# Optimization experiments

Hardware: AMD Instinct MI355X
Metric: run time of the kernel (lower is better)

The kernel has to match this reference:

```python
import jax, jax.numpy as jnp
import numpy as np

# Module hyperparameters (from init_kwargs)
LATENT = 1024
H = 16          # num query heads
HK = 4          # num key/value heads (GQA)
D = 64          # head_dim
CAUSAL = True
QKV_OUT = (3 * H + 2 * HK) * D  # 3584, as defined in the source module


def setup_inputs() -> dict:
    key = jax.random.key(0)
    k1, k2, k3 = jax.random.split(key, 3)
    B, S = 2, 2048
    x = jax.random.normal(k1, (B, S, LATENT), dtype=jnp.float32)
    # nn.Linear weights are [out_features, in_features]; scale like torch default init
    w_qkv = jax.random.normal(k2, (QKV_OUT, LATENT), dtype=jnp.float32) / np.sqrt(LATENT)
    w_out = jax.random.normal(k3, (LATENT, H * D), dtype=jnp.float32) / np.sqrt(H * D)
    return {"x": x, "w_qkv": w_qkv, "w_out": w_out}


def reference(x, w_qkv, w_out):
    B, S, _ = x.shape
    scale = 1.0 / np.sqrt(D).astype(np.float32)

    # Fused QKV projection: [B,S,(3H+2HK)*D]
    qkv = jnp.einsum('bsl,ol->bso', x, w_qkv)

    # Split: q takes H heads, k and v take HK heads each (GQA).
    # (The extra 2*H*D columns of the fused projection are allocated by the
    #  source module but unused by q/k/v, matching its layer sizing.)
    q = qkv[..., : H * D].reshape(B, S, H, D)
    k = qkv[..., H * D:(H + HK) * D].reshape(B, S, HK, D)
    v = qkv[..., (H + HK) * D:(H + 2 * HK) * D].reshape(B, S, HK, D)

    # Expand KV heads to match query heads (group factor H // HK)
    rep = H // HK
    k = jnp.repeat(k, rep, axis=2)  # [B,S,H,D]
    v = jnp.repeat(v, rep, axis=2)

    # Scaled dot-product attention
    scores = jnp.einsum('bshd,bthd->bhst', q, k) * scale  # [B,H,S,S]
    if CAUSAL:
        causal_mask = jnp.tril(jnp.ones((S, S), dtype=bool))
        scores = jnp.where(causal_mask, scores, jnp.finfo(scores.dtype).min)
    attn = jax.nn.softmax(scores, axis=-1)
    out = jnp.einsum('bhst,bthd->bshd', attn, v).reshape(B, S, H * D)

    # Output projection back to latent_size
    return jnp.einsum('bso,lo->bsl', out, w_out)
```

## Files before the change

### kernel.cpp

```cpp
#include <hip/hip_runtime.h>
#include <hip/hip_bf16.h>
#include <math.h>

typedef __attribute__((ext_vector_type(8))) short bf16x8;
typedef __attribute__((ext_vector_type(4))) float f32x4;
typedef unsigned short u16;
typedef unsigned int   u32;

#define DEVINL __device__ __forceinline__

DEVINL u16 f2bf(float x) {
    u32 u = __float_as_uint(x);
    u += 0x7fffu + ((u >> 16) & 1u);
    return (u16)(u >> 16);
}

DEVINL void gl_lds16(const void* g, void* s) {
    __builtin_amdgcn_global_load_lds(
        (const __attribute__((address_space(1))) u32*)g,
        (__attribute__((address_space(3))) u32*)s,
        16, 0, 0);
}

DEVINL f32x4 mfma16(bf16x8 a, bf16x8 b, f32x4 c) {
    return __builtin_amdgcn_mfma_f32_16x16x32_bf16(a, b, c, 0, 0, 0);
}

__global__ void cvt3(const float* __restrict__ x, const float* __restrict__ wq,
                     const float* __restrict__ wo,
                     u16* __restrict__ xb, u16* __restrict__ wqb, u16* __restrict__ wob) {
    int i = blockIdx.x * 256 + threadIdx.x;
    const float* s; u16* d; int j;
    if (i < 1048576)      { s = x;  d = xb;  j = i; }
    else if (i < 1441792) { s = wq; d = wqb; j = i - 1048576; }
    else                  { s = wo; d = wob; j = i - 1441792; }
    float4 v = ((const float4*)s)[j];
    ushort4 o;
    o.x = f2bf(v.x); o.y = f2bf(v.y); o.z = f2bf(v.z); o.w = f2bf(v.w);
    ((ushort4*)d)[j] = o;
}

template<int EP>
__launch_bounds__(256)
__global__ void gemm128(const u16* __restrict__ A, const u16* __restrict__ B,
                        const int N, const int K,
                        float* __restrict__ Cf,
                        u16* __restrict__ Qo, u16* __restrict__ Ko, u16* __restrict__ Vo)
{
    __shared__ __align__(16) u16 As[2][128 * 64];
    __shared__ __align__(16) u16 Bs[2][128 * 64];
    const int tid  = threadIdx.x;
    const int lane = tid & 63;
    const int quad = lane >> 4;
    const int lcol = lane & 15;
    const int w    = tid >> 6;
    const int wr   = w >> 1, wc = w & 1;
    const int lr   = lane >> 3;
    const int lc   = lane & 7;
    const int swst = lc ^ lr;
    const int rk   = lcol & 7;
    const int m0 = blockIdx.y * 128;
    const int n0 = blockIdx.x * 128;

    f32x4 acc[4][4];
    for (int mb = 0; mb < 4; mb++)
        for (int nb = 0; nb < 4; nb++)
            for (int i = 0; i < 4; i++) acc[mb][nb][i] = 0.f;

    const u16* Ap = A + (m0 + w * 8 + lr) * K + swst * 8;
    const u16* Bp = B + (n0 + w * 8 + lr) * K + swst * 8;

    for (int j = 0; j < 4; j++) {
        gl_lds16(Ap + j * 32 * K, &As[0][(j * 32 + w * 8) * 64]);
        gl_lds16(Bp + j * 32 * K, &Bs[0][(j * 32 + w * 8) * 64]);
    }
    __syncthreads();

    int cur = 0;
    for (int k0 = 0; k0 < K; k0 += 64) {
        if (k0 + 64 < K) {
            for (int j = 0; j < 4; j++) {
                gl_lds16(Ap + j * 32 * K + k0 + 64, &As[cur ^ 1][(j * 32 + w * 8) * 64]);
                gl_lds16(Bp + j * 32 * K + k0 + 64, &Bs[cur ^ 1][(j * 32 + w * 8) * 64]);
            }
        }
        for (int ks = 0; ks < 2; ks++) {
            const int ch = ((ks * 4 + quad) ^ rk) * 8;
            bf16x8 af[4], bf[4];
            for (int mb = 0; mb < 4; mb++)
                af[mb] = *(const bf16x8*)&As[cur][(wr * 64 + mb * 16 + lcol) * 64 + ch];
            for (int nb = 0; nb < 4; nb++)
                bf[nb] = *(const bf16x8*)&Bs[cur][(wc * 64 + nb * 16 + lcol) * 64 + ch];
            for (int mb = 0; mb < 4; mb++)
                for (int nb = 0; nb < 4; nb++)
                    acc[mb][nb] = mfma16(af[mb], bf[nb], acc[mb][nb]);
        }
        __syncthreads();
        cur ^= 1;
    }

    if (EP == 0) {
        for (int mb = 0; mb < 4; mb++)
            for (int nb = 0; nb < 4; nb++) {
                int row = m0 + wr * 64 + mb * 16 + quad * 4;
                int col = n0 + wc * 64 + nb * 16 + lcol;
                for (int i = 0; i < 4; i++)
                    Cf[(row + i) * N + col] = acc[mb][nb][i];
            }
    } else {
        const float qsc = 0.18033688011112042f;
        for (int mb = 0; mb < 4; mb++)
            for (int nb = 0; nb < 4; nb++)
                for (int i = 0; i < 4; i++) {
                    int row = m0 + wr * 64 + mb * 16 + quad * 4 + i;
                    int col = n0 + wc * 64 + nb * 16 + lcol;
                    int bb = row >> 11, ss = row & 2047;
                    if (col < 1024) {
                        int hh = col >> 6, dd = col & 63;
                        Qo[((bb * 16 + hh) * 2048 + ss) * 64 + dd] = f2bf(acc[mb][nb][i] * qsc);
                    } else if (col < 1280) {
                        int c = col - 1024, hh = c >> 6, dd = c & 63;
                        Ko[((bb * 4 + hh) * 2048 + ss) * 64 + dd] = f2bf(acc[mb][nb][i]);
                    } else {
                        int c = col - 1280, hh = c >> 6, dd = c & 63;
                        Vo[((bb * 4 + hh) * 64 + dd) * 2048 + ss] = f2bf(acc[mb][nb][i]);
                    }
                }
    }
}

__launch_bounds__(512, 4)
__global__ void attn_kernel(const u16* __restrict__ Qg, const u16* __restrict__ Kg,
                            const u16* __restrict__ Vtg, u16* __restrict__ Og)
{
    __shared__ __align__(16) u16 Ks[2][2][64 * 64];
    __shared__ __align__(16) u16 Vs[2][2][64 * 64];
    __shared__ __align__(16) u16 Ps[2][64 * 64];

    const int tid  = threadIdx.x;
    const int lane = tid & 63;
    const int w8   = tid >> 6;
    const int gpp  = w8 >> 2;
    const int wg   = w8 & 3;
    const int quad = lane >> 4;
    const int lcol = lane & 15;
    const int lr   = lane >> 3;
    const int lc   = lane & 7;
    const int swst = lc ^ lr;
    const int rk   = lcol & 7;
    const int hl   = lcol >> 3;

    const int p  = blockIdx.x;
    const int h  = blockIdx.y;
    const int b  = blockIdx.z;
    const int hk = h >> 2;

    const u16* Qp = Qg  + (b * 16 + h) * 2048 * 64;
    const u16* Kp = Kg  + (b * 4 + hk) * 2048 * 64;
    const u16* Vp = Vtg + (b * 4 + hk) * 64 * 2048;

    const int p0 = (wg * 16 + quad * 4) * 64 + ((hl ^ ((quad & 1) << 2)) << 3) + lc;

    float* Ob = (float*)(&Ks[1][0][0]);
    float* Lb = (float*)(&Vs[1][0][0]);

    for (int pass = 0; pass < 2; pass++) {
        const int qi = pass ? (31 - p) : p;
        const int q0 = qi * 64;
        const int nt = qi + 1;
        const int nIter = (nt + 1) >> 1;

        bf16x8 aqr[2];
        for (int ks = 0; ks < 2; ks++)
            aqr[ks] = *(const bf16x8*)(Qp + (q0 + wg * 16 + lcol) * 64 + ks * 32 + quad * 8);

        if (gpp < nt) {
            for (int j = 0; j < 2; j++) {
                const int r = wg * 16 + j * 8 + lr;
                gl_lds16(Kp + (gpp * 64 + r) * 64 + swst * 8, &Ks[gpp][0][wg * 1024 + j * 512]);
                gl_lds16(Vp + r * 2048 + gpp * 64 + swst * 8, &Vs[gpp][0][wg * 1024 + j * 512]);
            }
        }

        f32x4 o[4];
        float l_p[4];
        for (int db = 0; db < 4; db++)
            for (int i = 0; i < 4; i++) o[db][i] = 0.f;
        for (int i = 0; i < 4; i++) l_p[i] = 0.f;

        __syncthreads();

        for (int it = 0; it < nIter; ++it) {
            const int cur = it & 1;
            const int ti  = 2 * it + gpp;
            const int tin = ti + 2;
            if (tin < nt) {
                const int nbuf = cur ^ 1;
                for (int j = 0; j < 2; j++) {
                    const int r = wg * 16 + j * 8 + lr;
                    gl_lds16(Kp + (tin * 64 + r) * 64 + swst * 8, &Ks[gpp][nbuf][wg * 1024 + j * 512]);
                    gl_lds16(Vp + r * 2048 + tin * 64 + swst * 8, &Vs[gpp][nbuf][wg * 1024 + j * 512]);
                }
            }
            if (ti < nt) {
                f32x4 s[4];
                for (int cb = 0; cb < 4; cb++)
                    for (int i = 0; i < 4; i++) s[cb][i] = 0.f;
                for (int ks = 0; ks < 2; ks++) {
                    const int chq = ((ks * 4 + quad) ^ rk) * 8;
                    for (int cb = 0; cb < 4; cb++) {
                        bf16x8 bk = *(const bf16x8*)&Ks[gpp][cur][(cb * 16 + lcol) * 64 + chq];
                        s[cb] = mfma16(aqr[ks], bk, s[cb]);
                    }
                }

                if (ti == nt - 1) {
                    for (int cb = 0; cb < 4; cb++)
                        for (int i = 0; i < 4; i++) {
                            const bool masked = (cb * 16 + lcol) > (wg * 16 + quad * 4 + i);
                            s[cb][i] = masked ? -INFINITY : s[cb][i];
                        }
                }

                for (int cb = 0; cb < 4; cb++)
                    for (int i = 0; i < 4; i++) {
                        const float pv = __builtin_amdgcn_exp2f(s[cb][i]);
                        s[cb][i] = pv;
                        l_p[i] += pv;
                    }

                for (int cb = 0; cb < 4; cb++)
                    for (int i = 0; i < 4; i++)
                        Ps[gpp][(p0 + i * 64) ^ (((cb * 2) ^ i) << 3)] =
                            (u16)(__float_as_uint(s[cb][i]) >> 16);

                for (int kt = 0; kt < 2; kt++) {
                    const int chp = ((kt * 4 + quad) ^ rk) * 8;
                    bf16x8 ap = *(const bf16x8*)&Ps[gpp][(wg * 16 + lcol) * 64 + chp];
                    for (int db = 0; db < 4; db++) {
                        bf16x8 bv = *(const bf16x8*)&Vs[gpp][cur][(db * 16 + lcol) * 64 + chp];
                        o[db] = mfma16(ap, bv, o[db]);
                    }
                }
            }
            __syncthreads();
        }

        float lrow[4];
        for (int i = 0; i < 4; i++) {
            float l = l_p[i];
            for (int x = 1; x < 16; x <<= 1) l += __shfl_xor(l, x);
            lrow[i] = l;
        }
        if (gpp == 1) {
            for (int i = 0; i < 4; i++) {
                const int row = wg * 16 + quad * 4 + i;
                for (int db = 0; db < 4; db++)
                    Ob[row * 64 + db * 16 + lcol] = o[db][i];
                if (lcol == 0) Lb[row] = lrow[i];
            }
        }
        __syncthreads();
        if (gpp == 0) {
            for (int i = 0; i < 4; i++) {
                const int row = wg * 16 + quad * 4 + i;
                const float inv = 1.0f / (lrow[i] + Lb[row]);
                const int srow = q0 + row;
                for (int db = 0; db < 4; db++) {
                    const float val = (o[db][i] + Ob[row * 64 + db * 16 + lcol]) * inv;
                    Og[(b * 2048 + srow) * 1024 + h * 64 + db * 16 + lcol] = f2bf(val);
                }
            }
        }
        __syncthreads();
    }
}

extern "C" void kernel_launch(void* const* d_in, const int* in_sizes, int n_in,
                              void* d_out, int out_size, void* d_ws, size_t ws_size,
                              hipStream_t stream) {
    const float* x     = (const float*)d_in[0];
    const float* w_qkv = (const float*)d_in[1];
    const float* w_out = (const float*)d_in[2];
    float* out = (float*)d_out;
    char* ws = (char*)d_ws;

    u16* xb  = (u16*)(ws);
    u16* wqb = (u16*)(ws + 8  * 1024 * 1024);
    u16* wob = (u16*)(ws + 11 * 1024 * 1024);
    u16* qb  = (u16*)(ws + 13 * 1024 * 1024);
    u16* kb  = (u16*)(ws + 21 * 1024 * 1024);
    u16* vtb = (u16*)(ws + 23 * 1024 * 1024);
    u16* aob = (u16*)(ws);

    cvt3<<<6656, 256, 0, stream>>>(x, w_qkv, w_out, xb, wqb, wob);

    gemm128<1><<<dim3(12, 32), 256, 0, stream>>>(xb, wqb, 1536, 1024,
                                                 nullptr, qb, kb, vtb);
    attn_kernel<<<dim3(16, 16, 2), 512, 0, stream>>>(qb, kb, vtb, aob);
    gemm128<0><<<dim3(8, 32), 256, 0, stream>>>(aob, wob, 1024, 1024,
                                                out, nullptr, nullptr, nullptr);
}
```

Measured before the change: 165.2 us.

## Shrink GEMM tiles to 64x128 with two waves and prioritize attention MFMAs

Both projection GEMMs now use 64x128 output tiles computed by 128-thread blocks of two waves, each wave owning a 64x64 sub-tile. This doubles the grid (768 and 512 blocks) to fill the 256 CUs better, at the cost of more redundant B-tile loads per output element. The attention kernel also raises wave priority around its two MFMA loops with s_setprio, aiming to overlap matrix work with the softmax and load phases of other waves.

```diff
diff --git a/kernel.cpp b/kernel.cpp
--- a/kernel.cpp
+++ b/kernel.cpp
@@ -41,25 +41,24 @@
 }
 
 template<int EP>
-__launch_bounds__(256)
-__global__ void gemm128(const u16* __restrict__ A, const u16* __restrict__ B,
-                        const int N, const int K,
-                        float* __restrict__ Cf,
-                        u16* __restrict__ Qo, u16* __restrict__ Ko, u16* __restrict__ Vo)
+__launch_bounds__(128)
+__global__ void gemm2w(const u16* __restrict__ A, const u16* __restrict__ B,
+                       const int N, const int K,
+                       float* __restrict__ Cf,
+                       u16* __restrict__ Qo, u16* __restrict__ Ko, u16* __restrict__ Vo)
 {
-    __shared__ __align__(16) u16 As[2][128 * 64];
+    __shared__ __align__(16) u16 As[2][64 * 64];
     __shared__ __align__(16) u16 Bs[2][128 * 64];
     const int tid  = threadIdx.x;
     const int lane = tid & 63;
+    const int w    = tid >> 6;
     const int quad = lane >> 4;
     const int lcol = lane & 15;
-    const int w    = tid >> 6;
-    const int wr   = w >> 1, wc = w & 1;
     const int lr   = lane >> 3;
     const int lc   = lane & 7;
     const int swst = lc ^ lr;
     const int rk   = lcol & 7;
-    const int m0 = blockIdx.y * 128;
+    const int m0 = blockIdx.y * 64;
     const int n0 = blockIdx.x * 128;
 
     f32x4 acc[4][4];
@@ -70,30 +69,30 @@
     const u16* Ap = A + (m0 + w * 8 + lr) * K + swst * 8;
     const u16* Bp = B + (n0 + w * 8 + lr) * K + swst * 8;
 
-    for (int j = 0; j < 4; j++) {
-        gl_lds16(Ap + j * 32 * K, &As[0][(j * 32 + w * 8) * 64]);
-        gl_lds16(Bp + j * 32 * K, &Bs[0][(j * 32 + w * 8) * 64]);
-    }
+    for (int j = 0; j < 4; j++)
+        gl_lds16(Ap + j * 16 * K, &As[0][(j * 16 + w * 8) * 64]);
+    for (int g = 0; g < 8; g++)
+        gl_lds16(Bp + g * 16 * K, &Bs[0][(g * 16 + w * 8) * 64]);
     __syncthreads();
 
     int cur = 0;
     for (int k0 = 0; k0 < K; k0 += 64) {
         if (k0 + 64 < K) {
-            for (int j = 0; j < 4; j++) {
-                gl_lds16(Ap + j * 32 * K + k0 + 64, &As[cur ^ 1][(j * 32 + w * 8) * 64]);
-                gl_lds16(Bp + j * 32 * K + k0 + 64, &Bs[cur ^ 1][(j * 32 + w * 8) * 64]);
-            }
+            for (int j = 0; j < 4; j++)
+                gl_lds16(Ap + j * 16 * K + k0 + 64, &As[cur ^ 1][(j * 16 + w * 8) * 64]);
+            for (int g = 0; g < 8; g++)
+                gl_lds16(Bp + g * 16 * K + k0 + 64, &Bs[cur ^ 1][(g * 16 + w * 8) * 64]);
         }
         for (int ks = 0; ks < 2; ks++) {
             const int ch = ((ks * 4 + quad) ^ rk) * 8;
-            bf16x8 af[4], bf[4];
+            bf16x8 af[4], bfv[4];
             for (int mb = 0; mb < 4; mb++)
-                af[mb] = *(const bf16x8*)&As[cur][(wr * 64 + mb * 16 + lcol) * 64 + ch];
+                af[mb] = *(const bf16x8*)&As[cur][(mb * 16 + lcol) * 64 + ch];
             for (int nb = 0; nb < 4; nb++)
-                bf[nb] = *(const bf16x8*)&Bs[cur][(wc * 64 + nb * 16 + lcol) * 64 + ch];
+                bfv[nb] = *(const bf16x8*)&Bs[cur][(w * 64 + nb * 16 + lcol) * 64 + ch];
             for (int mb = 0; mb < 4; mb++)
                 for (int nb = 0; nb < 4; nb++)
-                    acc[mb][nb] = mfma16(af[mb], bf[nb], acc[mb][nb]);
+                    acc[mb][nb] = mfma16(af[mb], bfv[nb], acc[mb][nb]);
         }
         __syncthreads();
         cur ^= 1;
@@ -102,8 +101,8 @@
     if (EP == 0) {
         for (int mb = 0; mb < 4; mb++)
             for (int nb = 0; nb < 4; nb++) {
-                int row = m0 + wr * 64 + mb * 16 + quad * 4;
-                int col = n0 + wc * 64 + nb * 16 + lcol;
+                int row = m0 + mb * 16 + quad * 4;
+                int col = n0 + w * 64 + nb * 16 + lcol;
                 for (int i = 0; i < 4; i++)
                     Cf[(row + i) * N + col] = acc[mb][nb][i];
             }
@@ -112,8 +111,8 @@
         for (int mb = 0; mb < 4; mb++)
             for (int nb = 0; nb < 4; nb++)
                 for (int i = 0; i < 4; i++) {
-                    int row = m0 + wr * 64 + mb * 16 + quad * 4 + i;
-                    int col = n0 + wc * 64 + nb * 16 + lcol;
+                    int row = m0 + mb * 16 + quad * 4 + i;
+                    int col = n0 + w * 64 + nb * 16 + lcol;
                     int bb = row >> 11, ss = row & 2047;
                     if (col < 1024) {
                         int hh = col >> 6, dd = col & 63;
@@ -206,6 +205,7 @@
                 f32x4 s[4];
                 for (int cb = 0; cb < 4; cb++)
                     for (int i = 0; i < 4; i++) s[cb][i] = 0.f;
+                __builtin_amdgcn_s_setprio(1);
                 for (int ks = 0; ks < 2; ks++) {
                     const int chq = ((ks * 4 + quad) ^ rk) * 8;
                     for (int cb = 0; cb < 4; cb++) {
@@ -213,6 +213,7 @@
                         s[cb] = mfma16(aqr[ks], bk, s[cb]);
                     }
                 }
+                __builtin_amdgcn_s_setprio(0);
 
                 if (ti == nt - 1) {
                     for (int cb = 0; cb < 4; cb++)
@@ -234,6 +235,7 @@
                         Ps[gpp][(p0 + i * 64) ^ (((cb * 2) ^ i) << 3)] =
                             (u16)(__float_as_uint(s[cb][i]) >> 16);
 
+                __builtin_amdgcn_s_setprio(1);
                 for (int kt = 0; kt < 2; kt++) {
                     const int chp = ((kt * 4 + quad) ^ rk) * 8;
                     bf16x8 ap = *(const bf16x8*)&Ps[gpp][(wg * 16 + lcol) * 64 + chp];
@@ -242,6 +244,7 @@
                         o[db] = mfma16(ap, bv, o[db]);
                     }
                 }
+                __builtin_amdgcn_s_setprio(0);
             }
             __syncthreads();
         }
@@ -295,9 +298,9 @@
 
     cvt3<<<6656, 256, 0, stream>>>(x, w_qkv, w_out, xb, wqb, wob);
 
-    gemm128<1><<<dim3(12, 32), 256, 0, stream>>>(xb, wqb, 1536, 1024,
-                                                 nullptr, qb, kb, vtb);
+    gemm2w<1><<<dim3(12, 64), 128, 0, stream>>>(xb, wqb, 1536, 1024,
+                                                nullptr, qb, kb, vtb);
     attn_kernel<<<dim3(16, 16, 2), 512, 0, stream>>>(qb, kb, vtb, aob);
-    gemm128<0><<<dim3(8, 32), 256, 0, stream>>>(aob, wob, 1024, 1024,
-                                                out, nullptr, nullptr, nullptr);
-}
+    gemm2w<0><<<dim3(8, 64), 128, 0, stream>>>(aob, wob, 1024, 1024,
+                                               out, nullptr, nullptr, nullptr);
+}
```

New measurement: 160.2 us. 1.03x faster.
